# Optimization experiments

Measured on AMD Instinct MI355X. Metric: run time of the kernel, lower is better.

The kernel has to match this reference:

```python
import jax, jax.numpy as jnp
import numpy as np

D_MODEL = 1024
NUM_HEADS = 16
HEAD_DIMS = D_MODEL // NUM_HEADS


def setup_inputs() -> dict:
    key = jax.random.key(0)
    k1, k2, k3, k4, k5 = jax.random.split(key, 5)
    B, S = 2, 2048
    x = jax.random.normal(k1, (B, S, D_MODEL), dtype=jnp.float32)
    mask = jnp.zeros((B, S, S), dtype=jnp.float32)  # additive float mask
    # torch Linear weights; stored as (in, out) so y = x @ W + b
    s_in = 1.0 / np.sqrt(D_MODEL)
    Wqkv = jax.random.uniform(k2, (D_MODEL, 3 * D_MODEL), jnp.float32, -s_in, s_in)
    bqkv = jax.random.uniform(k3, (3 * D_MODEL,), jnp.float32, -s_in, s_in)
    Wo = jax.random.uniform(k4, (D_MODEL, D_MODEL), jnp.float32, -s_in, s_in)
    bo = jax.random.uniform(k5, (D_MODEL,), jnp.float32, -s_in, s_in)
    return {"x": x, "mask": mask, "Wqkv": Wqkv, "bqkv": bqkv, "Wo": Wo, "bo": bo}


def reference(x, mask, Wqkv, bqkv, Wo, bo):
    B, S, _ = x.shape
    qkv = x @ Wqkv + bqkv                                   # [B, S, 3*D]
    qkv = qkv.reshape(B, S, NUM_HEADS, 3 * HEAD_DIMS)
    qkv = jnp.transpose(qkv, (0, 2, 1, 3))                  # [B, H, S, 3*hd]
    q, k, v = jnp.split(qkv, 3, axis=-1)                    # each [B, H, S, hd]
    scale = 1.0 / np.sqrt(HEAD_DIMS).astype(np.float32)
    scores = jnp.einsum("bhqd,bhkd->bhqk", q, k) * scale    # [B, H, S, S]
    scores = scores + mask[:, None, :, :]
    attn = jax.nn.softmax(scores, axis=-1)
    values = jnp.einsum("bhqk,bhkd->bhqd", attn, v)         # [B, H, S, hd]
    # Faithful to original: direct row-major reshape (B,H,S,hd)->(B,S,H*hd),
    # WITHOUT transposing heads back (replicates the source's reshape).
    values = values.reshape(B, S, NUM_HEADS * HEAD_DIMS)
    out = values @ Wo + bo
    return out
```

## Files before the change

kernel.cpp:

```cpp
#include <hip/hip_runtime.h>
#include <stdint.h>


#define LOG2E 1.44269504088896340736f

typedef __attribute__((ext_vector_type(4))) float f32x4;
typedef __attribute__((ext_vector_type(8))) short short8v;
typedef __attribute__((ext_vector_type(8))) __bf16 bf16x8;

__device__ __forceinline__ unsigned short f2bf(float f) {
  unsigned u = __builtin_bit_cast(unsigned, f);
  u += 0x7FFFu + ((u >> 16) & 1u);
  return (unsigned short)(u >> 16);
}

__device__ __forceinline__ unsigned pack2(float lo, float hi) {
  return (unsigned)f2bf(lo) | ((unsigned)f2bf(hi) << 16);
}

__device__ __forceinline__ f32x4 mfma16(short8v a, short8v b, f32x4 c) {
  return __builtin_amdgcn_mfma_f32_16x16x32_bf16(
      __builtin_bit_cast(bf16x8, a), __builtin_bit_cast(bf16x8, b), c, 0, 0, 0);
}

__device__ __forceinline__ void gload_lds16(const void* g, void* l) {
  __builtin_amdgcn_global_load_lds(
      (const __attribute__((address_space(1))) void*)(uintptr_t)g,
      (__attribute__((address_space(3))) void*)(uintptr_t)l, 16, 0, 0);
}

__global__ void cvt_x_kernel(const float4* __restrict__ src,
                             uint2* __restrict__ dst, int n4) {
  int i = blockIdx.x * 256 + threadIdx.x;
  if (i < n4) {
    float4 v = src[i];
    dst[i] = make_uint2(pack2(v.x, v.y), pack2(v.z, v.w));
  }
}

__global__ void transpose_cvt_kernel(const float* __restrict__ src,
                                     unsigned short* __restrict__ dst,
                                     int R, int C) {
  __shared__ unsigned short tile[64][65];
  int tc = threadIdx.x & 63;
  int tr = threadIdx.x >> 6;
  int c0 = blockIdx.x * 64;
  int r0 = blockIdx.y * 64;
#pragma unroll
  for (int i = 0; i < 16; ++i) {
    int r = tr * 16 + i;
    tile[r][tc] = f2bf(src[(size_t)(r0 + r) * C + c0 + tc]);
  }
  __syncthreads();
#pragma unroll
  for (int i = 0; i < 16; ++i) {
    int cc = tr * 16 + i;
    dst[(size_t)(c0 + cc) * R + r0 + tc] = tile[tc][cc];
  }
}

__global__ __launch_bounds__(256, 2)
void gemm_qkv_kernel(const unsigned short* __restrict__ xbf,
                     const unsigned short* __restrict__ WT,
                     const float* __restrict__ bias,
                     unsigned short* __restrict__ Qb,
                     unsigned short* __restrict__ Kb,
                     unsigned short* __restrict__ VbT) {
  const int K = 1024;
  __shared__ __align__(16) unsigned short As[128 * 64];
  __shared__ __align__(16) unsigned short Bs[128 * 64];
  int tid = threadIdx.x;
  int lane = tid & 63;
  int wid = tid >> 6;
  int m0 = blockIdx.y * 128;
  int n0 = blockIdx.x * 128;
  int wm = (wid >> 1) * 64;
  int wn = (wid & 1) * 64;
  f32x4 acc[4][4] = {};
  for (int k0 = 0; k0 < K; k0 += 64) {
#pragma unroll
    for (int it = 0; it < 4; ++it) {
      int G = it * 256 + tid;
      int r = G >> 3, g = G & 7;
      int sg = g ^ (r & 7);
      gload_lds16(xbf + (size_t)(m0 + r) * K + k0 + sg * 8, &As[G * 8]);
      gload_lds16(WT + (size_t)(n0 + r) * K + k0 + sg * 8, &Bs[G * 8]);
    }
    __syncthreads();
#pragma unroll
    for (int ks = 0; ks < 2; ++ks) {
      short8v a[4], bf[4];
      int kg = ks * 4 + (lane >> 4);
#pragma unroll
      for (int i = 0; i < 4; ++i) {
        int ra = wm + i * 16 + (lane & 15);
        a[i] = *(const short8v*)&As[ra * 64 + ((kg ^ (ra & 7)) << 3)];
        int rb = wn + i * 16 + (lane & 15);
        bf[i] = *(const short8v*)&Bs[rb * 64 + ((kg ^ (rb & 7)) << 3)];
      }
#pragma unroll
      for (int i = 0; i < 4; ++i)
#pragma unroll
        for (int j = 0; j < 4; ++j)
          acc[i][j] = mfma16(a[i], bf[j], acc[i][j]);
    }
    __syncthreads();
  }
#pragma unroll
  for (int i = 0; i < 4; ++i) {
#pragma unroll
    for (int j = 0; j < 4; ++j) {
      int n = n0 + wn + j * 16 + (lane & 15);
      float bv = bias[n];
      int h = n / 192;
      int rr = n - h * 192;
      int t = rr >> 6;
      int d = rr & 63;
#pragma unroll
      for (int rg = 0; rg < 4; ++rg) {
        int m = m0 + wm + i * 16 + ((lane >> 4) << 2) + rg;
        int b = m >> 11, s = m & 2047;
        unsigned short val = f2bf(acc[i][j][rg] + bv);
        int bh = b * 16 + h;
        if (t == 2) {
          VbT[((size_t)bh * 64 + d) * 2048 + s] = val;
        } else {
          unsigned short* dst = (t == 0) ? Qb : Kb;
          dst[((size_t)bh * 2048 + s) * 64 + d] = val;
        }
      }
    }
  }
}


#define ATTN_STAGE(kt_, bi_)                                                  \
  do {                                                                        \
    _Pragma("unroll") for (int it_ = 0; it_ < 2; ++it_) {                     \
      int G_ = it_ * 256 + tid;                                               \
      int r_ = G_ >> 3, g_ = G_ & 7;                                          \
      int sg_ = g_ ^ (r_ & 7);                                                \
      gload_lds16(Kb + bh_off + (size_t)((kt_)*64 + r_) * 64 + sg_ * 8,       \
                  &Ks[bi_][G_ * 8]);                                          \
      gload_lds16(VbT + bh_off + (size_t)r_ * 2048 + (kt_)*64 + sg_ * 8,      \
                  &Vs[bi_][G_ * 8]);                                          \
    }                                                                         \
  } while (0)

#define ATTN_TILE(kt_, CUR_)                                                  \
  do {                                                                        \
    if ((kt_) < 31) ATTN_STAGE((kt_) + 1, (CUR_) ^ 1);                        \
           \
    const float* mp_ = mrow + (size_t)(kt_)*64;                               \
    float mk_[4][4];                                                          \
    _Pragma("unroll") for (int f = 0; f < 4; ++f)                             \
        _Pragma("unroll") for (int r = 0; r < 4; ++r)                         \
            mk_[f][r] = mp_[(size_t)r * 2048 + f * 16];                       \
                    \
    f32x4 sf[4] = {};                                                         \
    _Pragma("unroll") for (int ks = 0; ks < 2; ++ks) {                        \
      short8v qa = ks ? qa1 : qa0;                                            \
      int kg = ks * 4 + (lane >> 4);                                          \
      _Pragma("unroll") for (int f = 0; f < 4; ++f) {                         \
        int row = f * 16 + (lane & 15);                                       \
        short8v kb =                                                          \
            *(const short8v*)&Ks[CUR_][row * 64 + ((kg ^ (row & 7)) << 3)];   \
        sf[f] = mfma16(qa, kb, sf[f]);                                        \
      }                                                                       \
    }                                                                         \
                                  \
    float mt_[4];                                                             \
    _Pragma("unroll") for (int f = 0; f < 4; ++f)                             \
        _Pragma("unroll") for (int r = 0; r < 4; ++r)                         \
            sf[f][r] = fmaf(sf[f][r], 0.125f, mk_[f][r]);                     \
    _Pragma("unroll") for (int r = 0; r < 4; ++r)                             \
        mt_[r] = fmaxf(fmaxf(sf[0][r], sf[1][r]), fmaxf(sf[2][r], sf[3][r])); \
    _Pragma("unroll") for (int xm = 1; xm < 16; xm <<= 1)                     \
        _Pragma("unroll") for (int r = 0; r < 4; ++r)                         \
            mt_[r] = fmaxf(mt_[r], __shfl_xor(mt_[r], xm));                   \
                 \
    bool ok_ = (mt_[0] <= m_run[0] + THR) && (mt_[1] <= m_run[1] + THR) &&    \
               (mt_[2] <= m_run[2] + THR) && (mt_[3] <= m_run[3] + THR);      \
    if (!__all(ok_)) {                                                        \
      _Pragma("unroll") for (int r = 0; r < 4; ++r) {                         \
        float mn_ = fmaxf(m_run[r], mt_[r]);                                  \
        float al_ = exp2f((m_run[r] - mn_) * LOG2E);                          \
        m_run[r] = mn_;                                                       \
        mL[r] = mn_ * LOG2E;                                                  \
        l_lane[r] *= al_;                                                     \
        _Pragma("unroll") for (int f = 0; f < 4; ++f) o[f][r] *= al_;         \
      }                                                                       \
    }                                                                         \
                       \
    unsigned short pb_[4][4];                                                 \
    _Pragma("unroll") for (int f = 0; f < 4; ++f)                             \
        _Pragma("unroll") for (int r = 0; r < 4; ++r) {                       \
      float p_ = exp2f(fmaf(sf[f][r], LOG2E, -mL[r]));                        \
      l_lane[r] += p_;                                                        \
      pb_[f][r] = f2bf(p_);                                                   \
    }                                                                         \
                \
    _Pragma("unroll") for (int f = 0; f < 4; ++f)                             \
        _Pragma("unroll") for (int r = 0; r < 4; ++r) {                       \
      int prow_ = ((lane >> 4) << 2) + r;                                     \
      int pcol_ = f * 16 + (lane & 15);                                       \
      Ps[wid][prow_ * 64 + (((pcol_ >> 3) ^ (prow_ & 7)) << 3) +              \
              (pcol_ & 7)] = pb_[f][r];                                       \
    }                                                                         \
                                 \
    _Pragma("unroll") for (int ks = 0; ks < 2; ++ks) {                        \
      int arow_ = lane & 15;                                                  \
      int kg = ks * 4 + (lane >> 4);                                          \
      short8v pa =                                                            \
          *(const short8v*)&Ps[wid][arow_ * 64 + ((kg ^ (arow_ & 7)) << 3)];  \
      _Pragma("unroll") for (int f = 0; f < 4; ++f) {                         \
        int vrow_ = f * 16 + (lane & 15);                                     \
        short8v vb =                                                          \
            *(const short8v*)&Vs[CUR_][vrow_ * 64 + ((kg ^ (vrow_ & 7)) << 3)]; \
        o[f] = mfma16(pa, vb, o[f]);                                          \
      }                                                                       \
    }                                                                         \
    __syncthreads();                                                          \
  } while (0)

__global__ __launch_bounds__(256, 4)
void attn_kernel(const unsigned short* __restrict__ Qb,
                 const unsigned short* __restrict__ Kb,
                 const unsigned short* __restrict__ VbT,
                 const float* __restrict__ mask,
                 unsigned short* __restrict__ vals) {
  __shared__ __align__(16) unsigned short Ks[2][64 * 64];
  __shared__ __align__(16) unsigned short Vs[2][64 * 64];
  __shared__ __align__(16) unsigned short Ps[4][16 * 64];
  int tid = threadIdx.x;
  int lane = tid & 63;
  int wid = tid >> 6;
  int h = blockIdx.x & 15;
  int qt = (blockIdx.x >> 4) & 31;
  int b = blockIdx.x >> 9;
  int bh = b * 16 + h;
  size_t bh_off = (size_t)bh * 2048 * 64;
  int q0 = qt * 64 + wid * 16;

  const unsigned short* qptr =
      Qb + bh_off + (size_t)(q0 + (lane & 15)) * 64 + ((lane >> 4) << 3);
  short8v qa0 = *(const short8v*)qptr;
  short8v qa1 = *(const short8v*)(qptr + 32);

  f32x4 o[4] = {};
  float m_run[4], l_lane[4], mL[4];
#pragma unroll
  for (int r = 0; r < 4; ++r) { m_run[r] = -1e30f; l_lane[r] = 0.f; mL[r] = 0.f; }

  const float* mrow =
      mask + ((size_t)b * 2048 + q0 + ((lane >> 4) << 2)) * 2048 + (lane & 15);

  const float THR = 4.0f;

  ATTN_STAGE(0, 0);
  __syncthreads();

  for (int t = 0; t < 16; ++t) {
    ATTN_TILE(2 * t, 0);
    ATTN_TILE(2 * t + 1, 1);
  }

#pragma unroll
  for (int xm = 1; xm < 16; xm <<= 1)
#pragma unroll
    for (int r = 0; r < 4; ++r) l_lane[r] += __shfl_xor(l_lane[r], xm);
  float rinv[4];
#pragma unroll
  for (int r = 0; r < 4; ++r) rinv[r] = 1.0f / l_lane[r];

#pragma unroll
  for (int f = 0; f < 4; ++f)
#pragma unroll
    for (int r = 0; r < 4; ++r) {
      int s = q0 + ((lane >> 4) << 2) + r;
      int d = f * 16 + (lane & 15);
      int s2 = h * 128 + (s >> 4);
      int c2 = ((s & 15) << 6) + d;
      vals[((size_t)b * 2048 + s2) * 1024 + c2] = f2bf(o[f][r] * rinv[r]);
    }
}

__global__ __launch_bounds__(256, 2)
void gemm_out_kernel(const unsigned short* __restrict__ vals,
                     const unsigned short* __restrict__ WoT,
                     const float* __restrict__ bo,
                     float* __restrict__ out) {
  const int K = 1024;
  __shared__ __align__(16) unsigned short As[128 * 64];
  __shared__ __align__(16) unsigned short Bs[128 * 64];
  int tid = threadIdx.x;
  int lane = tid & 63;
  int wid = tid >> 6;
  int m0 = blockIdx.y * 128;
  int n0 = blockIdx.x * 128;
  int wm = (wid >> 1) * 64;
  int wn = (wid & 1) * 64;
  f32x4 acc[4][4] = {};
  for (int k0 = 0; k0 < K; k0 += 64) {
#pragma unroll
    for (int it = 0; it < 4; ++it) {
      int G = it * 256 + tid;
      int r = G >> 3, g = G & 7;
      int sg = g ^ (r & 7);
      gload_lds16(vals + (size_t)(m0 + r) * K + k0 + sg * 8, &As[G * 8]);
      gload_lds16(WoT + (size_t)(n0 + r) * K + k0 + sg * 8, &Bs[G * 8]);
    }
    __syncthreads();
#pragma unroll
    for (int ks = 0; ks < 2; ++ks) {
      short8v a[4], bf[4];
      int kg = ks * 4 + (lane >> 4);
#pragma unroll
      for (int i = 0; i < 4; ++i) {
        int ra = wm + i * 16 + (lane & 15);
        a[i] = *(const short8v*)&As[ra * 64 + ((kg ^ (ra & 7)) << 3)];
        int rb = wn + i * 16 + (lane & 15);
        bf[i] = *(const short8v*)&Bs[rb * 64 + ((kg ^ (rb & 7)) << 3)];
      }
#pragma unroll
      for (int i = 0; i < 4; ++i)
#pragma unroll
        for (int j = 0; j < 4; ++j)
          acc[i][j] = mfma16(a[i], bf[j], acc[i][j]);
    }
    __syncthreads();
  }
#pragma unroll
  for (int i = 0; i < 4; ++i) {
#pragma unroll
    for (int j = 0; j < 4; ++j) {
      int n = n0 + wn + j * 16 + (lane & 15);
      float bv = bo[n];
#pragma unroll
      for (int rg = 0; rg < 4; ++rg) {
        int m = m0 + wm + i * 16 + ((lane >> 4) << 2) + rg;
        out[(size_t)m * 1024 + n] = acc[i][j][rg] + bv;
      }
    }
  }
}

extern "C" void kernel_launch(void* const* d_in, const int* in_sizes, int n_in,
                              void* d_out, int out_size, void* d_ws,
                              size_t ws_size, hipStream_t stream) {
  const float* x    = (const float*)d_in[0];
  const float* mask = (const float*)d_in[1];
  const float* Wqkv = (const float*)d_in[2];
  const float* bqkv = (const float*)d_in[3];
  const float* Wo   = (const float*)d_in[4];
  const float* bo   = (const float*)d_in[5];
  float* out = (float*)d_out;

  char* ws = (char*)d_ws;
  unsigned short* xbf   = (unsigned short*)(ws);
  unsigned short* WqkvT = (unsigned short*)(ws + 8388608);
  unsigned short* WoT   = (unsigned short*)(ws + 14680064);
  unsigned short* Qb    = (unsigned short*)(ws + 16777216);
  unsigned short* Kb    = (unsigned short*)(ws + 25165824);
  unsigned short* VbT   = (unsigned short*)(ws + 33554432);
  unsigned short* vals  = xbf;

  hipLaunchKernelGGL(cvt_x_kernel, dim3(4096), dim3(256), 0, stream,
                     (const float4*)x, (uint2*)xbf, 1048576);
  hipLaunchKernelGGL(transpose_cvt_kernel, dim3(48, 16), dim3(256), 0, stream,
                     Wqkv, WqkvT, 1024, 3072);
  hipLaunchKernelGGL(transpose_cvt_kernel, dim3(16, 16), dim3(256), 0, stream,
                     Wo, WoT, 1024, 1024);
  hipLaunchKernelGGL(gemm_qkv_kernel, dim3(24, 32), dim3(256), 0, stream,
                     xbf, WqkvT, bqkv, Qb, Kb, VbT);
  hipLaunchKernelGGL(attn_kernel, dim3(1024), dim3(256), 0, stream,
                     Qb, Kb, VbT, mask, vals);
  hipLaunchKernelGGL(gemm_out_kernel, dim3(8, 32), dim3(256), 0, stream,
                     vals, WoT, bo, out);
}
```

Measured before the change: 276.9 us.

## Compute transposed S tile to keep P in registers, dropping LDS round-trip

Swaps the MFMA operands so each lane holds a column of the score tile (one query row per lane). P can then be packed straight into the A operand of the PV MFMA without going through shared memory. Row max and sum now take two cross-lane shuffles instead of four per row, and mask loads become vectorized float4 reads. V is read as two 4-element halves to match the permuted k ordering, which adds some LDS instructions and shuffles to broadcast the rescale factors.

```diff
diff --git a/kernel.cpp b/kernel.cpp
--- a/kernel.cpp
+++ b/kernel.cpp
@@ -6,7 +6,10 @@
 
 typedef __attribute__((ext_vector_type(4))) float f32x4;
 typedef __attribute__((ext_vector_type(8))) short short8v;
+typedef __attribute__((ext_vector_type(4))) short short4v;
 typedef __attribute__((ext_vector_type(8))) __bf16 bf16x8;
+typedef __attribute__((ext_vector_type(2))) __bf16 bf16x2;
+typedef __attribute__((ext_vector_type(4))) unsigned uint4v;
 
 __device__ __forceinline__ unsigned short f2bf(float f) {
   unsigned u = __builtin_bit_cast(unsigned, f);
@@ -16,6 +19,13 @@
 
 __device__ __forceinline__ unsigned pack2(float lo, float hi) {
   return (unsigned)f2bf(lo) | ((unsigned)f2bf(hi) << 16);
+}
+
+__device__ __forceinline__ unsigned packbf(float lo, float hi) {
+  bf16x2 t;
+  t[0] = (__bf16)lo;
+  t[1] = (__bf16)hi;
+  return __builtin_bit_cast(unsigned, t);
 }
 
 __device__ __forceinline__ f32x4 mfma16(short8v a, short8v b, f32x4 c) {
@@ -150,74 +160,82 @@
 #define ATTN_TILE(kt_, CUR_)                                                  \
   do {                                                                        \
     if ((kt_) < 31) ATTN_STAGE((kt_) + 1, (CUR_) ^ 1);                        \
-           \
-    const float* mp_ = mrow + (size_t)(kt_)*64;                               \
-    float mk_[4][4];                                                          \
+                \
+    f32x4 mk_[4];                                                             \
     _Pragma("unroll") for (int f = 0; f < 4; ++f)                             \
-        _Pragma("unroll") for (int r = 0; r < 4; ++r)                         \
-            mk_[f][r] = mp_[(size_t)r * 2048 + f * 16];                       \
-                    \
+        mk_[f] = *(const f32x4*)(mrowq + (size_t)(kt_)*64 + f * 16);          \
+                            \
     f32x4 sf[4] = {};                                                         \
     _Pragma("unroll") for (int ks = 0; ks < 2; ++ks) {                        \
       short8v qa = ks ? qa1 : qa0;                                            \
-      int kg = ks * 4 + (lane >> 4);                                          \
+      int kg = ks * 4 + hi;                                                   \
       _Pragma("unroll") for (int f = 0; f < 4; ++f) {                         \
-        int row = f * 16 + (lane & 15);                                       \
+        int row = f * 16 + lq;                                                \
         short8v kb =                                                          \
             *(const short8v*)&Ks[CUR_][row * 64 + ((kg ^ (row & 7)) << 3)];   \
-        sf[f] = mfma16(qa, kb, sf[f]);                                        \
+        sf[f] = mfma16(kb, qa, sf[f]);                                        \
       }                                                                       \
     }                                                                         \
-                                  \
-    float mt_[4];                                                             \
     _Pragma("unroll") for (int f = 0; f < 4; ++f)                             \
         _Pragma("unroll") for (int r = 0; r < 4; ++r)                         \
             sf[f][r] = fmaf(sf[f][r], 0.125f, mk_[f][r]);                     \
-    _Pragma("unroll") for (int r = 0; r < 4; ++r)                             \
-        mt_[r] = fmaxf(fmaxf(sf[0][r], sf[1][r]), fmaxf(sf[2][r], sf[3][r])); \
-    _Pragma("unroll") for (int xm = 1; xm < 16; xm <<= 1)                     \
-        _Pragma("unroll") for (int r = 0; r < 4; ++r)                         \
-            mt_[r] = fmaxf(mt_[r], __shfl_xor(mt_[r], xm));                   \
                  \
-    bool ok_ = (mt_[0] <= m_run[0] + THR) && (mt_[1] <= m_run[1] + THR) &&    \
-               (mt_[2] <= m_run[2] + THR) && (mt_[3] <= m_run[3] + THR);      \
-    if (!__all(ok_)) {                                                        \
-      _Pragma("unroll") for (int r = 0; r < 4; ++r) {                         \
-        float mn_ = fmaxf(m_run[r], mt_[r]);                                  \
-        float al_ = exp2f((m_run[r] - mn_) * LOG2E);                          \
-        m_run[r] = mn_;                                                       \
-        mL[r] = mn_ * LOG2E;                                                  \
-        l_lane[r] *= al_;                                                     \
-        _Pragma("unroll") for (int f = 0; f < 4; ++f) o[f][r] *= al_;         \
+    float mx0_ = fmaxf(fmaxf(sf[0][0], sf[0][1]), fmaxf(sf[0][2], sf[0][3])); \
+    float mx1_ = fmaxf(fmaxf(sf[1][0], sf[1][1]), fmaxf(sf[1][2], sf[1][3])); \
+    float mx2_ = fmaxf(fmaxf(sf[2][0], sf[2][1]), fmaxf(sf[2][2], sf[2][3])); \
+    float mx3_ = fmaxf(fmaxf(sf[3][0], sf[3][1]), fmaxf(sf[3][2], sf[3][3])); \
+    float mt_ = fmaxf(fmaxf(mx0_, mx1_), fmaxf(mx2_, mx3_));                  \
+    mt_ = fmaxf(mt_, __shfl_xor(mt_, 16));                                    \
+    mt_ = fmaxf(mt_, __shfl_xor(mt_, 32));                                    \
+                                                               \
+    if (!__all(mt_ <= m_s + THR)) {                                           \
+      float mn_ = fmaxf(m_s, mt_);                                            \
+      float al_ = exp2f((m_s - mn_) * LOG2E);                                 \
+      m_s = mn_;                                                              \
+      mLs = mn_ * LOG2E;                                                      \
+      l_s *= al_;                                                             \
+      float a0_ = __shfl(al_, (lane & 48) | hi4);                             \
+      float a1_ = __shfl(al_, (lane & 48) | (hi4 + 1));                       \
+      float a2_ = __shfl(al_, (lane & 48) | (hi4 + 2));                       \
+      float a3_ = __shfl(al_, (lane & 48) | (hi4 + 3));                       \
+      _Pragma("unroll") for (int f = 0; f < 4; ++f) {                         \
+        o[f][0] *= a0_; o[f][1] *= a1_; o[f][2] *= a2_; o[f][3] *= a3_;       \
       }                                                                       \
     }                                                                         \
-                       \
-    unsigned short pb_[4][4];                                                 \
-    _Pragma("unroll") for (int f = 0; f < 4; ++f)                             \
-        _Pragma("unroll") for (int r = 0; r < 4; ++r) {                       \
-      float p_ = exp2f(fmaf(sf[f][r], LOG2E, -mL[r]));                        \
-      l_lane[r] += p_;                                                        \
-      pb_[f][r] = f2bf(p_);                                                   \
-    }                                                                         \
-                \
-    _Pragma("unroll") for (int f = 0; f < 4; ++f)                             \
-        _Pragma("unroll") for (int r = 0; r < 4; ++r) {                       \
-      int prow_ = ((lane >> 4) << 2) + r;                                     \
-      int pcol_ = f * 16 + (lane & 15);                                       \
-      Ps[wid][prow_ * 64 + (((pcol_ >> 3) ^ (prow_ & 7)) << 3) +              \
-              (pcol_ & 7)] = pb_[f][r];                                       \
-    }                                                                         \
-                                 \
+            \
+    unsigned pk_[4][2];                                                       \
+    _Pragma("unroll") for (int f = 0; f < 4; ++f) {                           \
+      float p0_ = exp2f(fmaf(sf[f][0], LOG2E, -mLs));                         \
+      float p1_ = exp2f(fmaf(sf[f][1], LOG2E, -mLs));                         \
+      float p2_ = exp2f(fmaf(sf[f][2], LOG2E, -mLs));                         \
+      float p3_ = exp2f(fmaf(sf[f][3], LOG2E, -mLs));                         \
+      l_s += (p0_ + p1_) + (p2_ + p3_);                                       \
+      pk_[f][0] = packbf(p0_, p1_);                                           \
+      pk_[f][1] = packbf(p2_, p3_);                                           \
+    }                                                                         \
+    \
+    \
     _Pragma("unroll") for (int ks = 0; ks < 2; ++ks) {                        \
-      int arow_ = lane & 15;                                                  \
-      int kg = ks * 4 + (lane >> 4);                                          \
-      short8v pa =                                                            \
-          *(const short8v*)&Ps[wid][arow_ * 64 + ((kg ^ (arow_ & 7)) << 3)];  \
+      uint4v au_;                                                             \
+      au_[0] = pk_[2 * ks][0];                                                \
+      au_[1] = pk_[2 * ks][1];                                                \
+      au_[2] = pk_[2 * ks + 1][0];                                            \
+      au_[3] = pk_[2 * ks + 1][1];                                            \
+      short8v pa = __builtin_bit_cast(short8v, au_);                          \
       _Pragma("unroll") for (int f = 0; f < 4; ++f) {                         \
-        int vrow_ = f * 16 + (lane & 15);                                     \
-        short8v vb =                                                          \
-            *(const short8v*)&Vs[CUR_][vrow_ * 64 + ((kg ^ (vrow_ & 7)) << 3)]; \
-        o[f] = mfma16(pa, vb, o[f]);                                          \
+        int vrow_ = f * 16 + lq;                                              \
+        int blkA_ = 4 * ks + (hi >> 1);                                       \
+        int eA_ = vrow_ * 64 + (((blkA_) ^ (vrow_ & 7)) << 3) +               \
+                  ((hi & 1) << 2);                                            \
+        int eB_ = vrow_ * 64 + (((blkA_ + 2) ^ (vrow_ & 7)) << 3) +           \
+                  ((hi & 1) << 2);                                            \
+        short4v vlo_ = *(const short4v*)&Vs[CUR_][eA_];                       \
+        short4v vhi_ = *(const short4v*)&Vs[CUR_][eB_];                       \
+        short8v vb_;                                                          \
+        vb_[0] = vlo_[0]; vb_[1] = vlo_[1]; vb_[2] = vlo_[2];                 \
+        vb_[3] = vlo_[3]; vb_[4] = vhi_[0]; vb_[5] = vhi_[1];                 \
+        vb_[6] = vhi_[2]; vb_[7] = vhi_[3];                                   \
+        o[f] = mfma16(pa, vb_, o[f]);                                         \
       }                                                                       \
     }                                                                         \
     __syncthreads();                                                          \
@@ -231,10 +249,12 @@
                  unsigned short* __restrict__ vals) {
   __shared__ __align__(16) unsigned short Ks[2][64 * 64];
   __shared__ __align__(16) unsigned short Vs[2][64 * 64];
-  __shared__ __align__(16) unsigned short Ps[4][16 * 64];
   int tid = threadIdx.x;
   int lane = tid & 63;
   int wid = tid >> 6;
+  int lq = lane & 15;
+  int hi = lane >> 4;
+  int hi4 = hi << 2;
   int h = blockIdx.x & 15;
   int qt = (blockIdx.x >> 4) & 31;
   int b = blockIdx.x >> 9;
@@ -243,17 +263,14 @@
   int q0 = qt * 64 + wid * 16;
 
   const unsigned short* qptr =
-      Qb + bh_off + (size_t)(q0 + (lane & 15)) * 64 + ((lane >> 4) << 3);
+      Qb + bh_off + (size_t)(q0 + lq) * 64 + (hi << 3);
   short8v qa0 = *(const short8v*)qptr;
   short8v qa1 = *(const short8v*)(qptr + 32);
 
   f32x4 o[4] = {};
-  float m_run[4], l_lane[4], mL[4];
-#pragma unroll
-  for (int r = 0; r < 4; ++r) { m_run[r] = -1e30f; l_lane[r] = 0.f; mL[r] = 0.f; }
-
-  const float* mrow =
-      mask + ((size_t)b * 2048 + q0 + ((lane >> 4) << 2)) * 2048 + (lane & 15);
+  float m_s = -1e30f, l_s = 0.f, mLs = 0.f;
+
+  const float* mrowq = mask + ((size_t)b * 2048 + q0 + lq) * 2048 + hi4;
 
   const float THR = 4.0f;
 
@@ -265,23 +282,22 @@
     ATTN_TILE(2 * t + 1, 1);
   }
 
-#pragma unroll
-  for (int xm = 1; xm < 16; xm <<= 1)
-#pragma unroll
-    for (int r = 0; r < 4; ++r) l_lane[r] += __shfl_xor(l_lane[r], xm);
-  float rinv[4];
-#pragma unroll
-  for (int r = 0; r < 4; ++r) rinv[r] = 1.0f / l_lane[r];
+  l_s += __shfl_xor(l_s, 16);
+  l_s += __shfl_xor(l_s, 32);
+  float ri_ = 1.0f / l_s;
+  float rv_[4];
+#pragma unroll
+  for (int r = 0; r < 4; ++r) rv_[r] = __shfl(ri_, (lane & 48) | (hi4 + r));
 
 #pragma unroll
   for (int f = 0; f < 4; ++f)
 #pragma unroll
     for (int r = 0; r < 4; ++r) {
-      int s = q0 + ((lane >> 4) << 2) + r;
-      int d = f * 16 + (lane & 15);
+      int s = q0 + hi4 + r;
+      int d = f * 16 + lq;
       int s2 = h * 128 + (s >> 4);
       int c2 = ((s & 15) << 6) + d;
-      vals[((size_t)b * 2048 + s2) * 1024 + c2] = f2bf(o[f][r] * rinv[r]);
+      vals[((size_t)b * 2048 + s2) * 1024 + c2] = f2bf(o[f][r] * rv_[r]);
     }
 }
 
```

Result: faster. 252.7 us (-8.7%).
